# Optimization experiments

Hardware: AMD Instinct MI355X
Metric: run time of the kernel (lower is better)

## Reference

```python
import jax, jax.numpy as jnp
import numpy as np

B, CQ, CK, H, W = 8, 256, 256, 96, 96
EPS = 1e-4
SLOPE = 0.01  # torch LeakyReLU default


def conv1x1(x, w, b):
    # x: [B,Ci,H,W], w: [Co,Ci], b: [Co]
    return jnp.einsum('oi,bihw->bohw', w, x) + b[None, :, None, None]


def setup_inputs() -> dict:
    key = jax.random.key(0)
    ks = jax.random.split(key, 8)
    s = 0.02  # weight init scale for numerical sanity
    return {
        'q': jax.random.normal(ks[0], (B, CQ, H, W), jnp.float32),
        'v': jax.random.normal(ks[1], (B, CK, H, W), jnp.float32),
        'Wq': jax.random.normal(ks[2], (CQ, CQ), jnp.float32) * s,
        'bq': jnp.zeros((CQ,), jnp.float32),
        'Wk': jax.random.normal(ks[3], (CK, CK), jnp.float32) * s,
        'bk': jnp.zeros((CK,), jnp.float32),
        'Wv': jax.random.normal(ks[4], (CK, CQ), jnp.float32) * s,
        'bv': jnp.zeros((CK,), jnp.float32),
        'bn_gamma': jnp.ones((CQ,), jnp.float32),
        'bn_beta': jnp.zeros((CQ,), jnp.float32),
        'bn_mean': jnp.zeros((CQ,), jnp.float32),
        'bn_var': jnp.ones((CQ,), jnp.float32),
        'Wo1': jax.random.normal(ks[5], (CQ, CQ), jnp.float32) * s,
        'bo1': jnp.zeros((CQ,), jnp.float32),
        'Wo2': jax.random.normal(ks[6], (CQ, CQ), jnp.float32) * s,
        'bo2': jnp.zeros((CQ,), jnp.float32),
    }


def reference(q, v, Wq, bq, Wk, bk, Wv, bv, bn_gamma, bn_beta, bn_mean, bn_var, Wo1, bo1, Wo2, bo2):
    N = H * W
    query = conv1x1(q, Wq, bq).reshape(B, CQ, N)   # [B,CQ,N]
    key_t = conv1x1(v, Wk, bk).reshape(B, CK, N)   # [B,CK,N]
    value = conv1x1(q, Wv, bv).reshape(B, CK, N)   # [B,CK,N]
    # channel-attention: scores over channels, spatial is the contraction axis
    scale = float(N) ** 0.5
    scores = jnp.einsum('bcn,bdn->bcd', query, key_t) / scale  # [B,CQ,CK]
    attn = jax.nn.softmax(scores, axis=-1)
    out = jnp.einsum('bcd,bdn->bcn', attn, value)  # [B,CQ,N]
    # faithful permute(0,2,1).contiguous().view(B,-1,H,W): raw reshape of [B,N,CQ]
    out = jnp.transpose(out, (0, 2, 1)).reshape(B, CQ, H, W)
    # conv_out: BN (inference) -> LeakyReLU -> 1x1 conv -> LeakyReLU -> 1x1 conv
    inv = jax.lax.rsqrt(bn_var + EPS)
    out = (out - bn_mean[None, :, None, None]) * (bn_gamma * inv)[None, :, None, None] + bn_beta[None, :, None, None]
    out = jnp.where(out >= 0, out, SLOPE * out)
    out = conv1x1(out, Wo1, bo1)
    out = jnp.where(out >= 0, out, SLOPE * out)
    out = conv1x1(out, Wo2, bo2)
    return out
```

## Files before the change

kernel.cpp:

```cpp
#include <hip/hip_runtime.h>
#include <hip/hip_bf16.h>
#include <stdint.h>

#define CH     256
#define NSP    9216
#define NBATCH 8
#define NSPLIT 8
#define KSEG   1152

typedef unsigned short ushort_t;
using f32x4  = __attribute__((ext_vector_type(4))) float;
using bf16x8 = __attribute__((ext_vector_type(8))) short;

__device__ __forceinline__ ushort_t f2b(float f) {
  union { float f; uint32_t u; } v; v.f = f;
  return (ushort_t)((v.u + 0x7FFFu + ((v.u >> 16) & 1u)) >> 16);
}

__device__ __forceinline__ uint32_t swz(uint32_t row, uint32_t byte) {
  return row * 128u + (byte ^ ((row & 7u) << 4));
}

__global__ void wconv_kernel(const float* __restrict__ w0, const float* __restrict__ w1,
                             const float* __restrict__ w2, const float* __restrict__ w3,
                             const float* __restrict__ w4, ushort_t* __restrict__ dst) {
  int i = blockIdx.x * 256 + threadIdx.x;
  int sel = i >> 16;
  int loc = i & 0xFFFF;
  const float* s = (sel == 0) ? w0 : (sel == 1) ? w1 : (sel == 2) ? w2 : (sel == 3) ? w3 : w4;
  dst[i] = f2b(s[loc]);
}

template<int NOUT, bool IN_F32, bool LRELU, bool OUT_F32>
__global__ __launch_bounds__(256)
void conv_gemm_kernel(const ushort_t* __restrict__ A0, const float* __restrict__ bias0,
                      void* __restrict__ dst0,
                      const ushort_t* __restrict__ A1, const float* __restrict__ bias1,
                      ushort_t* __restrict__ dst1,
                      const void* __restrict__ srcv) {
  const int b    = blockIdx.y;
  const int n0   = blockIdx.x * 64;
  const int tid  = threadIdx.x;
  const int lane = tid & 63;
  const int w    = tid >> 6;

  __shared__ __align__(16) unsigned char sA0[256 * 128];
  __shared__ __align__(16) unsigned char sA1[(NOUT == 2) ? 256 * 128 : 16];
  __shared__ __align__(16) unsigned char sB[64 * 128];

  f32x4 acc0[4][4];
  f32x4 acc1[4][4];
  #pragma unroll
  for (int i = 0; i < 4; ++i)
    #pragma unroll
    for (int j = 0; j < 4; ++j)
      #pragma unroll
      for (int r = 0; r < 4; ++r) { acc0[i][j][r] = 0.f; acc1[i][j][r] = 0.f; }

  for (int kc = 0; kc < 4; ++kc) {
    const int k0 = kc * 64;
    #pragma unroll
    for (int it = 0; it < 8; ++it) {
      int slot = it * 256 + tid;
      int row  = slot >> 3;
      int seg  = slot & 7;
      uint4 d0 = *reinterpret_cast<const uint4*>(A0 + row * CH + k0 + seg * 8);
      *reinterpret_cast<uint4*>(&sA0[swz(row, seg * 16)]) = d0;
      if constexpr (NOUT == 2) {
        uint4 d1 = *reinterpret_cast<const uint4*>(A1 + row * CH + k0 + seg * 8);
        *reinterpret_cast<uint4*>(&sA1[swz(row, seg * 16)]) = d1;
      }
    }
    if constexpr (IN_F32) {
      const float* src = (const float*)srcv;
      #pragma unroll
      for (int r = 0; r < 4; ++r) {
        int ci = (tid >> 4) + r * 16;
        int nl = (tid & 15) * 4;
        float4 vv = *reinterpret_cast<const float4*>(
            src + ((size_t)b * CH + (k0 + ci)) * NSP + n0 + nl);
        float fv[4] = {vv.x, vv.y, vv.z, vv.w};
        #pragma unroll
        for (int j = 0; j < 4; ++j) {
          int jj = (j + (tid & 3)) & 3;
          *reinterpret_cast<ushort_t*>(&sB[swz(nl + jj, ci * 2)]) = f2b(fv[jj]);
        }
      }
    } else {
      const ushort_t* src = (const ushort_t*)srcv;
      #pragma unroll
      for (int r = 0; r < 2; ++r) {
        int ci = (tid >> 3) + r * 32;
        int nl = (tid & 7) * 8;
        uint4 dv = *reinterpret_cast<const uint4*>(
            src + ((size_t)b * CH + (k0 + ci)) * NSP + n0 + nl);
        const ushort_t* hv = reinterpret_cast<const ushort_t*>(&dv);
        #pragma unroll
        for (int j = 0; j < 8; ++j) {
          int jj = (j + (tid & 7)) & 7;
          *reinterpret_cast<ushort_t*>(&sB[swz(nl + jj, ci * 2)]) = hv[jj];
        }
      }
    }
    __syncthreads();
    #pragma unroll
    for (int ks = 0; ks < 2; ++ks) {
      const int kb = ks * 64 + (lane >> 4) * 16;
      bf16x8 fb[4], fa0[4];
      #pragma unroll
      for (int ni = 0; ni < 4; ++ni)
        fb[ni] = *reinterpret_cast<const bf16x8*>(&sB[swz(ni * 16 + (lane & 15), kb)]);
      #pragma unroll
      for (int mi = 0; mi < 4; ++mi)
        fa0[mi] = *reinterpret_cast<const bf16x8*>(&sA0[swz(w * 64 + mi * 16 + (lane & 15), kb)]);
      #pragma unroll
      for (int mi = 0; mi < 4; ++mi)
        #pragma unroll
        for (int ni = 0; ni < 4; ++ni)
          acc0[mi][ni] = __builtin_amdgcn_mfma_f32_16x16x32_bf16(fa0[mi], fb[ni], acc0[mi][ni], 0, 0, 0);
      if constexpr (NOUT == 2) {
        bf16x8 fa1[4];
        #pragma unroll
        for (int mi = 0; mi < 4; ++mi)
          fa1[mi] = *reinterpret_cast<const bf16x8*>(&sA1[swz(w * 64 + mi * 16 + (lane & 15), kb)]);
        #pragma unroll
        for (int mi = 0; mi < 4; ++mi)
          #pragma unroll
          for (int ni = 0; ni < 4; ++ni)
            acc1[mi][ni] = __builtin_amdgcn_mfma_f32_16x16x32_bf16(fa1[mi], fb[ni], acc1[mi][ni], 0, 0, 0);
      }
    }
    __syncthreads();
  }
  #pragma unroll
  for (int mi = 0; mi < 4; ++mi) {
    const int coB = w * 64 + mi * 16 + ((lane >> 4) << 2);
    #pragma unroll
    for (int ni = 0; ni < 4; ++ni) {
      const int n = n0 + ni * 16 + (lane & 15);
      #pragma unroll
      for (int r = 0; r < 4; ++r) {
        const int co = coB + r;
        const size_t oidx = ((size_t)b * CH + co) * NSP + n;
        float x = acc0[mi][ni][r] + bias0[co];
        if constexpr (LRELU) x = (x >= 0.f) ? x : 0.01f * x;
        if constexpr (OUT_F32) ((float*)dst0)[oidx] = x;
        else                   ((ushort_t*)dst0)[oidx] = f2b(x);
        if constexpr (NOUT == 2) {
          float y = acc1[mi][ni][r] + bias1[co];
          dst1[oidx] = f2b(y);
        }
      }
    }
  }
}

__global__ __launch_bounds__(256)
void scores_kernel(const ushort_t* __restrict__ qry, const ushort_t* __restrict__ key,
                   float* __restrict__ part) {
  const int b  = blockIdx.z;
  const int s  = blockIdx.y;
  const int c0 = (blockIdx.x >> 1) * 128;
  const int d0 = (blockIdx.x & 1) * 128;
  const int tid  = threadIdx.x;
  const int lane = tid & 63;
  const int wm = (tid >> 7) & 1;
  const int wn = (tid >> 6) & 1;

  __shared__ __align__(16) unsigned char sQ[128 * 128];
  __shared__ __align__(16) unsigned char sK[128 * 128];

  f32x4 acc[4][4];
  #pragma unroll
  for (int i = 0; i < 4; ++i)
    #pragma unroll
    for (int j = 0; j < 4; ++j)
      #pragma unroll
      for (int r = 0; r < 4; ++r) acc[i][j][r] = 0.f;

  for (int kc = 0; kc < KSEG / 64; ++kc) {
    const int k0 = s * KSEG + kc * 64;
    #pragma unroll
    for (int it = 0; it < 4; ++it) {
      int slot = it * 256 + tid;
      int row  = slot >> 3;
      int seg  = slot & 7;
      *reinterpret_cast<uint4*>(&sQ[swz(row, seg * 16)]) =
          *reinterpret_cast<const uint4*>(qry + ((size_t)b * CH + c0 + row) * NSP + k0 + seg * 8);
      *reinterpret_cast<uint4*>(&sK[swz(row, seg * 16)]) =
          *reinterpret_cast<const uint4*>(key + ((size_t)b * CH + d0 + row) * NSP + k0 + seg * 8);
    }
    __syncthreads();
    #pragma unroll
    for (int ks = 0; ks < 2; ++ks) {
      const int kb = ks * 64 + (lane >> 4) * 16;
      bf16x8 fq[4], fk[4];
      #pragma unroll
      for (int mi = 0; mi < 4; ++mi)
        fq[mi] = *reinterpret_cast<const bf16x8*>(&sQ[swz(wm * 64 + mi * 16 + (lane & 15), kb)]);
      #pragma unroll
      for (int ni = 0; ni < 4; ++ni)
        fk[ni] = *reinterpret_cast<const bf16x8*>(&sK[swz(wn * 64 + ni * 16 + (lane & 15), kb)]);
      #pragma unroll
      for (int mi = 0; mi < 4; ++mi)
        #pragma unroll
        for (int ni = 0; ni < 4; ++ni)
          acc[mi][ni] = __builtin_amdgcn_mfma_f32_16x16x32_bf16(fq[mi], fk[ni], acc[mi][ni], 0, 0, 0);
    }
    __syncthreads();
  }
  const size_t base = ((size_t)b * NSPLIT + s) * CH;
  #pragma unroll
  for (int mi = 0; mi < 4; ++mi) {
    #pragma unroll
    for (int ni = 0; ni < 4; ++ni) {
      #pragma unroll
      for (int r = 0; r < 4; ++r) {
        int c = c0 + wm * 64 + mi * 16 + ((lane >> 4) << 2) + r;
        int d = d0 + wn * 64 + ni * 16 + (lane & 15);
        part[(base + c) * CH + d] = acc[mi][ni][r];
      }
    }
  }
}

__global__ __launch_bounds__(64)
void softmax_kernel(const float* __restrict__ part, ushort_t* __restrict__ attn) {
  const int c = blockIdx.x;
  const int b = blockIdx.y;
  const int lane = threadIdx.x;
  float sv[4] = {0.f, 0.f, 0.f, 0.f};
  for (int sp = 0; sp < NSPLIT; ++sp) {
    const float* p = part + (((size_t)b * NSPLIT + sp) * CH + c) * CH;
    #pragma unroll
    for (int r = 0; r < 4; ++r) sv[r] += p[r * 64 + lane];
  }
  #pragma unroll
  for (int r = 0; r < 4; ++r) sv[r] *= (1.0f / 96.0f);
  float m = fmaxf(fmaxf(sv[0], sv[1]), fmaxf(sv[2], sv[3]));
  for (int off = 32; off > 0; off >>= 1) m = fmaxf(m, __shfl_xor(m, off));
  float e[4]; float sum = 0.f;
  #pragma unroll
  for (int r = 0; r < 4; ++r) { e[r] = expf(sv[r] - m); sum += e[r]; }
  for (int off = 32; off > 0; off >>= 1) sum += __shfl_xor(sum, off);
  float inv = 1.0f / sum;
  ushort_t* ap = attn + ((size_t)b * CH + c) * CH;
  #pragma unroll
  for (int r = 0; r < 4; ++r) ap[r * 64 + lane] = f2b(e[r] * inv);
}

__global__ __launch_bounds__(256)
void attnout_kernel(const ushort_t* __restrict__ attn, const ushort_t* __restrict__ val,
                    const float* __restrict__ gamma, const float* __restrict__ beta,
                    const float* __restrict__ mean, const float* __restrict__ var,
                    ushort_t* __restrict__ tbuf) {
  const int b    = blockIdx.y;
  const int n0   = blockIdx.x * 64;
  const int tid  = threadIdx.x;
  const int lane = tid & 63;
  const int w    = tid >> 6;

  __shared__ __align__(16) unsigned char sm[64 * 260 * 4];
  unsigned char* sA = sm;
  unsigned char* sB = sm + 32768;

  f32x4 acc[4][4];
  #pragma unroll
  for (int i = 0; i < 4; ++i)
    #pragma unroll
    for (int j = 0; j < 4; ++j)
      #pragma unroll
      for (int r = 0; r < 4; ++r) acc[i][j][r] = 0.f;

  for (int kc = 0; kc < 4; ++kc) {
    const int k0 = kc * 64;
    #pragma unroll
    for (int it = 0; it < 8; ++it) {
      int slot = it * 256 + tid;
      int row  = slot >> 3;
      int seg  = slot & 7;
      *reinterpret_cast<uint4*>(&sA[swz(row, seg * 16)]) =
          *reinterpret_cast<const uint4*>(attn + ((size_t)b * CH + row) * CH + k0 + seg * 8);
    }
    #pragma unroll
    for (int r = 0; r < 2; ++r) {
      int dl = (tid >> 3) + r * 32;
      int nl = (tid & 7) * 8;
      uint4 dv = *reinterpret_cast<const uint4*>(
          val + ((size_t)b * CH + (k0 + dl)) * NSP + n0 + nl);
      const ushort_t* hv = reinterpret_cast<const ushort_t*>(&dv);
      #pragma unroll
      for (int j = 0; j < 8; ++j) {
        int jj = (j + (tid & 7)) & 7;
        *reinterpret_cast<ushort_t*>(&sB[swz(nl + jj, dl * 2)]) = hv[jj];
      }
    }
    __syncthreads();
    #pragma unroll
    for (int ks = 0; ks < 2; ++ks) {
      const int kb = ks * 64 + (lane >> 4) * 16;
      bf16x8 fb[4], fa[4];
      #pragma unroll
      for (int ni = 0; ni < 4; ++ni)
        fb[ni] = *reinterpret_cast<const bf16x8*>(&sB[swz(ni * 16 + (lane & 15), kb)]);
      #pragma unroll
      for (int mi = 0; mi < 4; ++mi)
        fa[mi] = *reinterpret_cast<const bf16x8*>(&sA[swz(w * 64 + mi * 16 + (lane & 15), kb)]);
      #pragma unroll
      for (int mi = 0; mi < 4; ++mi)
        #pragma unroll
        for (int ni = 0; ni < 4; ++ni)
          acc[mi][ni] = __builtin_amdgcn_mfma_f32_16x16x32_bf16(fa[mi], fb[ni], acc[mi][ni], 0, 0, 0);
    }
    __syncthreads();
  }
  float* eL = reinterpret_cast<float*>(sm);
  #pragma unroll
  for (int mi = 0; mi < 4; ++mi) {
    #pragma unroll
    for (int ni = 0; ni < 4; ++ni) {
      #pragma unroll
      for (int r = 0; r < 4; ++r) {
        int c  = w * 64 + mi * 16 + ((lane >> 4) << 2) + r;
        int nl = ni * 16 + (lane & 15);
        eL[nl * 260 + c] = acc[mi][ni][r];
      }
    }
  }
  __syncthreads();
  const int ml = tid & 63;
  const int c0 = (tid >> 6) * 64;
  const int m  = n0 + ml;
  const int cp = m / 36;
  const int npb = (m % 36) * 256 + c0;
  const float kf = gamma[cp] * rsqrtf(var[cp] + 1e-4f);
  const float bb = beta[cp] - mean[cp] * kf;
  ushort_t* op = tbuf + ((size_t)b * CH + cp) * NSP + npb;
  #pragma unroll
  for (int j = 0; j < 64; j += 4) {
    float4 xv = *reinterpret_cast<const float4*>(&eL[ml * 260 + c0 + j]);
    float x[4] = {xv.x, xv.y, xv.z, xv.w};
    #pragma unroll
    for (int t = 0; t < 4; ++t) {
      x[t] = x[t] * kf + bb;
      x[t] = (x[t] >= 0.f) ? x[t] : 0.01f * x[t];
    }
    uint2 pk;
    pk.x = (uint32_t)f2b(x[0]) | ((uint32_t)f2b(x[1]) << 16);
    pk.y = (uint32_t)f2b(x[2]) | ((uint32_t)f2b(x[3]) << 16);
    *reinterpret_cast<uint2*>(op + j) = pk;
  }
}

extern "C" void kernel_launch(void* const* d_in, const int* in_sizes, int n_in,
                              void* d_out, int out_size, void* d_ws, size_t ws_size,
                              hipStream_t stream) {
  (void)in_sizes; (void)n_in; (void)out_size; (void)ws_size;
  const float* q   = (const float*)d_in[0];
  const float* v   = (const float*)d_in[1];
  const float* Wq  = (const float*)d_in[2];
  const float* bq  = (const float*)d_in[3];
  const float* Wk  = (const float*)d_in[4];
  const float* bk  = (const float*)d_in[5];
  const float* Wv  = (const float*)d_in[6];
  const float* bv  = (const float*)d_in[7];
  const float* bng = (const float*)d_in[8];
  const float* bnb = (const float*)d_in[9];
  const float* bnm = (const float*)d_in[10];
  const float* bnv = (const float*)d_in[11];
  const float* Wo1 = (const float*)d_in[12];
  const float* bo1 = (const float*)d_in[13];
  const float* Wo2 = (const float*)d_in[14];
  const float* bo2 = (const float*)d_in[15];

  char* ws = (char*)d_ws;
  ushort_t* wq_b  = (ushort_t*)(ws);
  ushort_t* wk_b  = (ushort_t*)(ws + 131072);
  ushort_t* wv_b  = (ushort_t*)(ws + 262144);
  ushort_t* wo1_b = (ushort_t*)(ws + 393216);
  ushort_t* wo2_b = (ushort_t*)(ws + 524288);
  ushort_t* val   = (ushort_t*)(ws + 655360);
  float*    part  = (float*)   (ws + 655360 + 37748736);
  ushort_t* attn  = (ushort_t*)(ws + 655360 + 37748736 + 16777216);
  ushort_t* o1    = val;
  ushort_t* qry   = (ushort_t*)d_out;
  ushort_t* key   = qry + 18874368;
  ushort_t* tbuf  = qry;

  wconv_kernel<<<1280, 256, 0, stream>>>(Wq, Wk, Wv, Wo1, Wo2, wq_b);

  dim3 g1(NSP / 64, NBATCH);
  conv_gemm_kernel<2, true, false, false><<<g1, 256, 0, stream>>>(
      wq_b, bq, (void*)qry, wv_b, bv, val, q);
  conv_gemm_kernel<1, true, false, false><<<g1, 256, 0, stream>>>(
      wk_b, bk, (void*)key, nullptr, nullptr, nullptr, v);

  scores_kernel<<<dim3(4, NSPLIT, NBATCH), 256, 0, stream>>>(qry, key, part);
  softmax_kernel<<<dim3(CH, NBATCH), 64, 0, stream>>>(part, attn);

  attnout_kernel<<<g1, 256, 0, stream>>>(attn, val, bng, bnb, bnm, bnv, tbuf);

  conv_gemm_kernel<1, false, true, false><<<g1, 256, 0, stream>>>(
      wo1_b, bo1, (void*)o1, nullptr, nullptr, nullptr, tbuf);
  conv_gemm_kernel<1, false, false, true><<<g1, 256, 0, stream>>>(
      wo2_b, bo2, d_out, nullptr, nullptr, nullptr, o1);
}
```

Before: 440.6 us.

## Fuse attention output, BN, and both output convs into one kernel

Replaces the attnout kernel and the two output 1x1 conv GEMMs with a single mega_kernel. It computes attn@value for a block of spatial positions, applies BN and LeakyReLU, then runs both output convs from LDS, so the two bf16 intermediate tensors never round-trip through global memory. Supporting changes: the weights are pre-swizzled so they can be copied straight into LDS with global_load_lds, the value projection is written in a transposed swizzled layout, and the projection kernel's input staging is vectorized. The mega kernel uses 104KB of LDS at 512 threads per block, which limits occupancy and adds tricky index mapping for the permute-reshape.

Result: faster. 403.2 us (-8.5%).

```diff
diff --git a/kernel.cpp b/kernel.cpp
--- a/kernel.cpp
+++ b/kernel.cpp
@@ -21,32 +21,53 @@
   return row * 128u + (byte ^ ((row & 7u) << 4));
 }
 
+typedef __attribute__((address_space(3))) void       lds_void;
+typedef const __attribute__((address_space(1))) void g_void;
+__device__ __forceinline__ void glds16(const void* g, void* l) {
+  __builtin_amdgcn_global_load_lds((g_void*)g, (lds_void*)l, 16, 0, 0);
+}
+
 __global__ void wconv_kernel(const float* __restrict__ w0, const float* __restrict__ w1,
                              const float* __restrict__ w2, const float* __restrict__ w3,
                              const float* __restrict__ w4, ushort_t* __restrict__ dst) {
-  int i = blockIdx.x * 256 + threadIdx.x;
-  int sel = i >> 16;
-  int loc = i & 0xFFFF;
-  const float* s = (sel == 0) ? w0 : (sel == 1) ? w1 : (sel == 2) ? w2 : (sel == 3) ? w3 : w4;
-  dst[i] = f2b(s[loc]);
-}
-
-template<int NOUT, bool IN_F32, bool LRELU, bool OUT_F32>
+  int gid = blockIdx.x * 256 + threadIdx.x;
+  int m   = gid >> 13;
+  int u   = gid & 8191;
+  const float* W = (m == 0) ? w0 : (m == 1) ? w1 : (m == 2) ? w2 : (m == 3) ? w3 : w4;
+  int lin = u * 16;
+  int kc  = lin >> 15;
+  int co  = (lin >> 7) & 255;
+  int bb0 = lin & 127;
+  int k0  = kc * 64 + ((bb0 ^ ((co & 7) << 4)) >> 1);
+  const float* srow = W + co * 256 + k0;
+  float4 a = *reinterpret_cast<const float4*>(srow);
+  float4 c = *reinterpret_cast<const float4*>(srow + 4);
+  ushort_t o[8] = {f2b(a.x), f2b(a.y), f2b(a.z), f2b(a.w),
+                   f2b(c.x), f2b(c.y), f2b(c.z), f2b(c.w)};
+  uint4 pk;
+  pk.x = (uint32_t)o[0] | ((uint32_t)o[1] << 16);
+  pk.y = (uint32_t)o[2] | ((uint32_t)o[3] << 16);
+  pk.z = (uint32_t)o[4] | ((uint32_t)o[5] << 16);
+  pk.w = (uint32_t)o[6] | ((uint32_t)o[7] << 16);
+  *reinterpret_cast<uint4*>(dst + m * 65536 + (lin >> 1)) = pk;
+}
+
+template<int NOUT>
 __global__ __launch_bounds__(256)
-void conv_gemm_kernel(const ushort_t* __restrict__ A0, const float* __restrict__ bias0,
-                      void* __restrict__ dst0,
-                      const ushort_t* __restrict__ A1, const float* __restrict__ bias1,
-                      ushort_t* __restrict__ dst1,
-                      const void* __restrict__ srcv) {
+void proj_kernel(const ushort_t* __restrict__ Asw0, const float* __restrict__ bias0,
+                 ushort_t* __restrict__ dst0,
+                 const ushort_t* __restrict__ Asw1, const float* __restrict__ bias1,
+                 char* __restrict__ valt,
+                 const float* __restrict__ src) {
   const int b    = blockIdx.y;
   const int n0   = blockIdx.x * 64;
   const int tid  = threadIdx.x;
   const int lane = tid & 63;
   const int w    = tid >> 6;
 
-  __shared__ __align__(16) unsigned char sA0[256 * 128];
-  __shared__ __align__(16) unsigned char sA1[(NOUT == 2) ? 256 * 128 : 16];
-  __shared__ __align__(16) unsigned char sB[64 * 128];
+  __shared__ __align__(16) unsigned char sA0[32768];
+  __shared__ __align__(16) unsigned char sA1[(NOUT == 2) ? 32768 : 16];
+  __shared__ __align__(16) unsigned char sB[8192];
 
   f32x4 acc0[4][4];
   f32x4 acc1[4][4];
@@ -59,47 +80,33 @@
 
   for (int kc = 0; kc < 4; ++kc) {
     const int k0 = kc * 64;
+    if (kc > 0) __syncthreads();
     #pragma unroll
     for (int it = 0; it < 8; ++it) {
-      int slot = it * 256 + tid;
-      int row  = slot >> 3;
-      int seg  = slot & 7;
-      uint4 d0 = *reinterpret_cast<const uint4*>(A0 + row * CH + k0 + seg * 8);
-      *reinterpret_cast<uint4*>(&sA0[swz(row, seg * 16)]) = d0;
-      if constexpr (NOUT == 2) {
-        uint4 d1 = *reinterpret_cast<const uint4*>(A1 + row * CH + k0 + seg * 8);
-        *reinterpret_cast<uint4*>(&sA1[swz(row, seg * 16)]) = d1;
-      }
-    }
-    if constexpr (IN_F32) {
-      const float* src = (const float*)srcv;
+      int seg = (it * 4 + w) * 1024;
+      glds16((const char*)Asw0 + kc * 32768 + seg + lane * 16,
+             (void*)(sA0 + seg));
+      if constexpr (NOUT == 2)
+        glds16((const char*)Asw1 + kc * 32768 + seg + lane * 16,
+               (void*)(sA1 + seg));
+    }
+    {
+      const int ci0 = (tid >> 4) * 4;
+      const int n4  = (tid & 15) * 4;
+      float xv[4][4];
       #pragma unroll
       for (int r = 0; r < 4; ++r) {
-        int ci = (tid >> 4) + r * 16;
-        int nl = (tid & 15) * 4;
-        float4 vv = *reinterpret_cast<const float4*>(
-            src + ((size_t)b * CH + (k0 + ci)) * NSP + n0 + nl);
-        float fv[4] = {vv.x, vv.y, vv.z, vv.w};
-        #pragma unroll
-        for (int j = 0; j < 4; ++j) {
-          int jj = (j + (tid & 3)) & 3;
-          *reinterpret_cast<ushort_t*>(&sB[swz(nl + jj, ci * 2)]) = f2b(fv[jj]);
-        }
-      }
-    } else {
-      const ushort_t* src = (const ushort_t*)srcv;
-      #pragma unroll
-      for (int r = 0; r < 2; ++r) {
-        int ci = (tid >> 3) + r * 32;
-        int nl = (tid & 7) * 8;
-        uint4 dv = *reinterpret_cast<const uint4*>(
-            src + ((size_t)b * CH + (k0 + ci)) * NSP + n0 + nl);
-        const ushort_t* hv = reinterpret_cast<const ushort_t*>(&dv);
-        #pragma unroll
-        for (int j = 0; j < 8; ++j) {
-          int jj = (j + (tid & 7)) & 7;
-          *reinterpret_cast<ushort_t*>(&sB[swz(nl + jj, ci * 2)]) = hv[jj];
-        }
+        float4 t4 = *reinterpret_cast<const float4*>(
+            src + ((size_t)b * CH + (k0 + ci0 + r)) * NSP + n0 + n4);
+        xv[r][0] = t4.x; xv[r][1] = t4.y; xv[r][2] = t4.z; xv[r][3] = t4.w;
+      }
+      #pragma unroll
+      for (int j = 0; j < 4; ++j) {
+        uint64_t pk = (uint64_t)f2b(xv[0][j])
+                    | ((uint64_t)f2b(xv[1][j]) << 16)
+                    | ((uint64_t)f2b(xv[2][j]) << 32)
+                    | ((uint64_t)f2b(xv[3][j]) << 48);
+        *reinterpret_cast<uint64_t*>(&sB[swz(n4 + j, ci0 * 2)]) = pk;
       }
     }
     __syncthreads();
@@ -130,7 +137,6 @@
             acc1[mi][ni] = __builtin_amdgcn_mfma_f32_16x16x32_bf16(fa1[mi], fb[ni], acc1[mi][ni], 0, 0, 0);
       }
     }
-    __syncthreads();
   }
   #pragma unroll
   for (int mi = 0; mi < 4; ++mi) {
@@ -141,16 +147,31 @@
       #pragma unroll
       for (int r = 0; r < 4; ++r) {
         const int co = coB + r;
-        const size_t oidx = ((size_t)b * CH + co) * NSP + n;
-        float x = acc0[mi][ni][r] + bias0[co];
-        if constexpr (LRELU) x = (x >= 0.f) ? x : 0.01f * x;
-        if constexpr (OUT_F32) ((float*)dst0)[oidx] = x;
-        else                   ((ushort_t*)dst0)[oidx] = f2b(x);
-        if constexpr (NOUT == 2) {
-          float y = acc1[mi][ni][r] + bias1[co];
-          dst1[oidx] = f2b(y);
-        }
-      }
+        dst0[((size_t)b * CH + co) * NSP + n] = f2b(acc0[mi][ni][r] + bias0[co]);
+      }
+    }
+  }
+  if constexpr (NOUT == 2) {
+    __syncthreads();
+    #pragma unroll
+    for (int mi = 0; mi < 4; ++mi) {
+      const int co0 = w * 64 + mi * 16 + ((lane >> 4) << 2);
+      #pragma unroll
+      for (int ni = 0; ni < 4; ++ni) {
+        const int nl = ni * 16 + (lane & 15);
+        uint64_t pk = (uint64_t)f2b(acc1[mi][ni][0] + bias1[co0])
+                    | ((uint64_t)f2b(acc1[mi][ni][1] + bias1[co0 + 1]) << 16)
+                    | ((uint64_t)f2b(acc1[mi][ni][2] + bias1[co0 + 2]) << 32)
+                    | ((uint64_t)f2b(acc1[mi][ni][3] + bias1[co0 + 3]) << 48);
+        *reinterpret_cast<uint64_t*>(&sA0[nl * 512 + ((co0 * 2) ^ ((nl & 7) << 4))]) = pk;
+      }
+    }
+    __syncthreads();
+    char* vb = valt + (size_t)b * (NSP * 512) + (size_t)n0 * 512;
+    #pragma unroll
+    for (int i = 0; i < 8; ++i) {
+      *reinterpret_cast<uint4*>(vb + tid * 128 + i * 16) =
+          *reinterpret_cast<const uint4*>(sA0 + tid * 128 + i * 16);
     }
   }
 }
@@ -249,106 +270,201 @@
   for (int r = 0; r < 4; ++r) ap[r * 64 + lane] = f2b(e[r] * inv);
 }
 
-__global__ __launch_bounds__(256)
-void attnout_kernel(const ushort_t* __restrict__ attn, const ushort_t* __restrict__ val,
-                    const float* __restrict__ gamma, const float* __restrict__ beta,
-                    const float* __restrict__ mean, const float* __restrict__ var,
-                    ushort_t* __restrict__ tbuf) {
+__global__ __launch_bounds__(512)
+void mega_kernel(const ushort_t* __restrict__ attn, const char* __restrict__ valt,
+                 const ushort_t* __restrict__ w1sw, const float* __restrict__ bo1,
+                 const ushort_t* __restrict__ w2sw, const float* __restrict__ bo2,
+                 const float* __restrict__ gamma, const float* __restrict__ beta,
+                 const float* __restrict__ mean,  const float* __restrict__ var,
+                 float* __restrict__ out) {
   const int b    = blockIdx.y;
-  const int n0   = blockIdx.x * 64;
+  const int s    = blockIdx.x >> 2;
+  const int c0   = (blockIdx.x & 3) * 64;
   const int tid  = threadIdx.x;
   const int lane = tid & 63;
   const int w    = tid >> 6;
 
-  __shared__ __align__(16) unsigned char sm[64 * 260 * 4];
-  unsigned char* sA = sm;
-  unsigned char* sB = sm + 32768;
-
-  f32x4 acc[4][4];
+  __shared__ __align__(16) unsigned char L[104 * 1024];
+  unsigned char* sS = L;
+  unsigned char* sV = L + 8192;
+  unsigned char* sT = L + 40960;
+  unsigned char* sW = L + 73728;
+  unsigned char* sO = L;
+
+  const ushort_t* attn_b = attn + (size_t)b * 65536;
+  const char*     vt_b   = valt + (size_t)b * (NSP * 512);
+
+  f32x4 acc[4][2];
   #pragma unroll
   for (int i = 0; i < 4; ++i)
     #pragma unroll
-    for (int j = 0; j < 4; ++j)
+    for (int j = 0; j < 2; ++j)
       #pragma unroll
       for (int r = 0; r < 4; ++r) acc[i][j][r] = 0.f;
 
   for (int kc = 0; kc < 4; ++kc) {
-    const int k0 = kc * 64;
-    #pragma unroll
-    for (int it = 0; it < 8; ++it) {
-      int slot = it * 256 + tid;
-      int row  = slot >> 3;
-      int seg  = slot & 7;
-      *reinterpret_cast<uint4*>(&sA[swz(row, seg * 16)]) =
-          *reinterpret_cast<const uint4*>(attn + ((size_t)b * CH + row) * CH + k0 + seg * 8);
-    }
-    #pragma unroll
-    for (int r = 0; r < 2; ++r) {
-      int dl = (tid >> 3) + r * 32;
-      int nl = (tid & 7) * 8;
+    if (kc > 0) __syncthreads();
+    {
+      int row = tid >> 3, seg = tid & 7;
+      *reinterpret_cast<uint4*>(&sS[swz(row, seg * 16)]) =
+          *reinterpret_cast<const uint4*>(attn_b + (c0 + row) * 256 + kc * 64 + seg * 8);
+    }
+    #pragma unroll
+    for (int it = 0; it < 4; ++it) {
+      int slot = it * 512 + tid;
+      int j = slot >> 3, seg = slot & 7;
+      int n = s + 36 * j;
       uint4 dv = *reinterpret_cast<const uint4*>(
-          val + ((size_t)b * CH + (k0 + dl)) * NSP + n0 + nl);
-      const ushort_t* hv = reinterpret_cast<const ushort_t*>(&dv);
-      #pragma unroll
-      for (int j = 0; j < 8; ++j) {
-        int jj = (j + (tid & 7)) & 7;
-        *reinterpret_cast<ushort_t*>(&sB[swz(nl + jj, dl * 2)]) = hv[jj];
-      }
+          vt_b + n * 512 + ((kc * 128 + seg * 16) ^ ((n & 7) << 4)));
+      *reinterpret_cast<uint4*>(&sV[swz(j, seg * 16)]) = dv;
     }
     __syncthreads();
     #pragma unroll
     for (int ks = 0; ks < 2; ++ks) {
       const int kb = ks * 64 + (lane >> 4) * 16;
-      bf16x8 fb[4], fa[4];
-      #pragma unroll
-      for (int ni = 0; ni < 4; ++ni)
-        fb[ni] = *reinterpret_cast<const bf16x8*>(&sB[swz(ni * 16 + (lane & 15), kb)]);
+      bf16x8 fa[4], fb[2];
       #pragma unroll
       for (int mi = 0; mi < 4; ++mi)
-        fa[mi] = *reinterpret_cast<const bf16x8*>(&sA[swz(w * 64 + mi * 16 + (lane & 15), kb)]);
+        fa[mi] = *reinterpret_cast<const bf16x8*>(&sS[swz(mi * 16 + (lane & 15), kb)]);
+      #pragma unroll
+      for (int ni = 0; ni < 2; ++ni)
+        fb[ni] = *reinterpret_cast<const bf16x8*>(&sV[swz(w * 32 + ni * 16 + (lane & 15), kb)]);
       #pragma unroll
       for (int mi = 0; mi < 4; ++mi)
         #pragma unroll
+        for (int ni = 0; ni < 2; ++ni)
+          acc[mi][ni] = __builtin_amdgcn_mfma_f32_16x16x32_bf16(fa[mi], fb[ni], acc[mi][ni], 0, 0, 0);
+    }
+  }
+  {
+    float kf[2], bb[2];
+    #pragma unroll
+    for (int ni = 0; ni < 2; ++ni) {
+      int j = w * 32 + ni * 16 + (lane & 15);
+      float iv = rsqrtf(var[j] + 1e-4f);
+      kf[ni] = gamma[j] * iv;
+      bb[ni] = beta[j] - mean[j] * kf[ni];
+    }
+    #pragma unroll
+    for (int mi = 0; mi < 4; ++mi)
+      #pragma unroll
+      for (int ni = 0; ni < 2; ++ni) {
+        int j = w * 32 + ni * 16 + (lane & 15);
+        #pragma unroll
+        for (int r = 0; r < 4; ++r) {
+          int cl = mi * 16 + ((lane >> 4) << 2) + r;
+          float x = acc[mi][ni][r] * kf[ni] + bb[ni];
+          x = (x >= 0.f) ? x : 0.01f * x;
+          *reinterpret_cast<ushort_t*>(&sT[cl * 512 + ((j * 2) ^ ((cl & 7) << 4))]) = f2b(x);
+        }
+      }
+  }
+  __syncthreads();
+
+  f32x4 a2[2][4];
+  #pragma unroll
+  for (int i = 0; i < 2; ++i)
+    #pragma unroll
+    for (int j = 0; j < 4; ++j)
+      #pragma unroll
+      for (int r = 0; r < 4; ++r) a2[i][j][r] = 0.f;
+
+  for (int kc = 0; kc < 4; ++kc) {
+    if (kc > 0) __syncthreads();
+    #pragma unroll
+    for (int it = 0; it < 4; ++it) {
+      int seg = (it * 8 + w) * 1024;
+      glds16((const char*)w1sw + kc * 32768 + seg + lane * 16, (void*)(sW + seg));
+    }
+    __syncthreads();
+    #pragma unroll
+    for (int ks = 0; ks < 2; ++ks) {
+      const int kbw = ks * 64 + (lane >> 4) * 16;
+      const int kbt = kc * 128 + kbw;
+      bf16x8 fa2[2], fb2[4];
+      #pragma unroll
+      for (int mi = 0; mi < 2; ++mi)
+        fa2[mi] = *reinterpret_cast<const bf16x8*>(&sW[swz(w * 32 + mi * 16 + (lane & 15), kbw)]);
+      #pragma unroll
+      for (int ni = 0; ni < 4; ++ni) {
+        int cl = ni * 16 + (lane & 15);
+        fb2[ni] = *reinterpret_cast<const bf16x8*>(&sT[cl * 512 + (kbt ^ ((cl & 7) << 4))]);
+      }
+      #pragma unroll
+      for (int mi = 0; mi < 2; ++mi)
+        #pragma unroll
         for (int ni = 0; ni < 4; ++ni)
-          acc[mi][ni] = __builtin_amdgcn_mfma_f32_16x16x32_bf16(fa[mi], fb[ni], acc[mi][ni], 0, 0, 0);
-    }
-    __syncthreads();
-  }
-  float* eL = reinterpret_cast<float*>(sm);
-  #pragma unroll
-  for (int mi = 0; mi < 4; ++mi) {
+          a2[mi][ni] = __builtin_amdgcn_mfma_f32_16x16x32_bf16(fa2[mi], fb2[ni], a2[mi][ni], 0, 0, 0);
+    }
+  }
+  #pragma unroll
+  for (int mi = 0; mi < 2; ++mi) {
+    const int co0 = w * 32 + mi * 16 + ((lane >> 4) << 2);
     #pragma unroll
     for (int ni = 0; ni < 4; ++ni) {
+      const int cl = ni * 16 + (lane & 15);
+      float y[4];
       #pragma unroll
       for (int r = 0; r < 4; ++r) {
-        int c  = w * 64 + mi * 16 + ((lane >> 4) << 2) + r;
-        int nl = ni * 16 + (lane & 15);
-        eL[nl * 260 + c] = acc[mi][ni][r];
-      }
+        y[r] = a2[mi][ni][r] + bo1[co0 + r];
+        y[r] = (y[r] >= 0.f) ? y[r] : 0.01f * y[r];
+      }
+      uint64_t pk = (uint64_t)f2b(y[0]) | ((uint64_t)f2b(y[1]) << 16)
+                  | ((uint64_t)f2b(y[2]) << 32) | ((uint64_t)f2b(y[3]) << 48);
+      *reinterpret_cast<uint64_t*>(&sO[cl * 512 + ((co0 * 2) ^ ((cl & 7) << 4))]) = pk;
     }
   }
   __syncthreads();
-  const int ml = tid & 63;
-  const int c0 = (tid >> 6) * 64;
-  const int m  = n0 + ml;
-  const int cp = m / 36;
-  const int npb = (m % 36) * 256 + c0;
-  const float kf = gamma[cp] * rsqrtf(var[cp] + 1e-4f);
-  const float bb = beta[cp] - mean[cp] * kf;
-  ushort_t* op = tbuf + ((size_t)b * CH + cp) * NSP + npb;
-  #pragma unroll
-  for (int j = 0; j < 64; j += 4) {
-    float4 xv = *reinterpret_cast<const float4*>(&eL[ml * 260 + c0 + j]);
-    float x[4] = {xv.x, xv.y, xv.z, xv.w};
-    #pragma unroll
-    for (int t = 0; t < 4; ++t) {
-      x[t] = x[t] * kf + bb;
-      x[t] = (x[t] >= 0.f) ? x[t] : 0.01f * x[t];
-    }
-    uint2 pk;
-    pk.x = (uint32_t)f2b(x[0]) | ((uint32_t)f2b(x[1]) << 16);
-    pk.y = (uint32_t)f2b(x[2]) | ((uint32_t)f2b(x[3]) << 16);
-    *reinterpret_cast<uint2*>(op + j) = pk;
+
+  f32x4 a3[2][4];
+  #pragma unroll
+  for (int i = 0; i < 2; ++i)
+    #pragma unroll
+    for (int j = 0; j < 4; ++j)
+      #pragma unroll
+      for (int r = 0; r < 4; ++r) a3[i][j][r] = 0.f;
+
+  for (int kc = 0; kc < 4; ++kc) {
+    if (kc > 0) __syncthreads();
+    #pragma unroll
+    for (int it = 0; it < 4; ++it) {
+      int seg = (it * 8 + w) * 1024;
+      glds16((const char*)w2sw + kc * 32768 + seg + lane * 16, (void*)(sW + seg));
+    }
+    __syncthreads();
+    #pragma unroll
+    for (int ks = 0; ks < 2; ++ks) {
+      const int kbw = ks * 64 + (lane >> 4) * 16;
+      const int kbt = kc * 128 + kbw;
+      bf16x8 fa3[2], fb3[4];
+      #pragma unroll
+      for (int mi = 0; mi < 2; ++mi)
+        fa3[mi] = *reinterpret_cast<const bf16x8*>(&sW[swz(w * 32 + mi * 16 + (lane & 15), kbw)]);
+      #pragma unroll
+      for (int ni = 0; ni < 4; ++ni) {
+        int cl = ni * 16 + (lane & 15);
+        fb3[ni] = *reinterpret_cast<const bf16x8*>(&sO[cl * 512 + (kbt ^ ((cl & 7) << 4))]);
+      }
+      #pragma unroll
+      for (int mi = 0; mi < 2; ++mi)
+        #pragma unroll
+        for (int ni = 0; ni < 4; ++ni)
+          a3[mi][ni] = __builtin_amdgcn_mfma_f32_16x16x32_bf16(fa3[mi], fb3[ni], a3[mi][ni], 0, 0, 0);
+    }
+  }
+  #pragma unroll
+  for (int mi = 0; mi < 2; ++mi) {
+    const int coB = w * 32 + mi * 16 + ((lane >> 4) << 2);
+    #pragma unroll
+    for (int ni = 0; ni < 4; ++ni) {
+      const int cl = ni * 16 + (lane & 15);
+      #pragma unroll
+      for (int r = 0; r < 4; ++r) {
+        const int co = coB + r;
+        out[(size_t)b * (CH * NSP) + (size_t)co * NSP + s * 256 + c0 + cl] =
+            a3[mi][ni][r] + bo2[co];
+      }
+    }
   }
 }
 
@@ -379,29 +495,21 @@
   ushort_t* wv_b  = (ushort_t*)(ws + 262144);
   ushort_t* wo1_b = (ushort_t*)(ws + 393216);
   ushort_t* wo2_b = (ushort_t*)(ws + 524288);
-  ushort_t* val   = (ushort_t*)(ws + 655360);
+  char*     valt  = ws + 655360;
   float*    part  = (float*)   (ws + 655360 + 37748736);
   ushort_t* attn  = (ushort_t*)(ws + 655360 + 37748736 + 16777216);
-  ushort_t* o1    = val;
   ushort_t* qry   = (ushort_t*)d_out;
   ushort_t* key   = qry + 18874368;
-  ushort_t* tbuf  = qry;
-
-  wconv_kernel<<<1280, 256, 0, stream>>>(Wq, Wk, Wv, Wo1, Wo2, wq_b);
+
+  wconv_kernel<<<160, 256, 0, stream>>>(Wq, Wk, Wv, Wo1, Wo2, wq_b);
 
   dim3 g1(NSP / 64, NBATCH);
-  conv_gemm_kernel<2, true, false, false><<<g1, 256, 0, stream>>>(
-      wq_b, bq, (void*)qry, wv_b, bv, val, q);
-  conv_gemm_kernel<1, true, false, false><<<g1, 256, 0, stream>>>(
-      wk_b, bk, (void*)key, nullptr, nullptr, nullptr, v);
+  proj_kernel<2><<<g1, 256, 0, stream>>>(wq_b, bq, qry, wv_b, bv, valt, q);
+  proj_kernel<1><<<g1, 256, 0, stream>>>(wk_b, bk, key, nullptr, nullptr, nullptr, v);
 
   scores_kernel<<<dim3(4, NSPLIT, NBATCH), 256, 0, stream>>>(qry, key, part);
   softmax_kernel<<<dim3(CH, NBATCH), 64, 0, stream>>>(part, attn);
 
-  attnout_kernel<<<g1, 256, 0, stream>>>(attn, val, bng, bnb, bnm, bnv, tbuf);
-
-  conv_gemm_kernel<1, false, true, false><<<g1, 256, 0, stream>>>(
-      wo1_b, bo1, (void*)o1, nullptr, nullptr, nullptr, tbuf);
-  conv_gemm_kernel<1, false, false, true><<<g1, 256, 0, stream>>>(
-      wo2_b, bo2, d_out, nullptr, nullptr, nullptr, o1);
-}
+  mega_kernel<<<dim3(144, NBATCH), 512, 0, stream>>>(
+      attn, valt, wo1_b, bo1, wo2_b, bo2, bng, bnb, bnm, bnv, (float*)d_out);
+}
```
